# Kernel optimization log

Hardware: AMD Instinct MI355X
Metric: run time of the kernel (lower is better)

## Reference

```python
import jax, jax.numpy as jnp
import numpy as np
import math

T = 2048; HID = 2048; H = 16; KV = 8; G = H // KV; D = 128
GH = 128; BS = 64; NB = T // BS
EPS = 1e-6; RATIO = 0.2; SCALE = 1.0 / math.sqrt(D)


def _rope_tables(length, dim, theta=1000000.0):
    inv = 1.0 / (theta ** (np.arange(0, dim, 2, dtype=np.float32) / dim))
    f = np.outer(np.arange(length, dtype=np.float32), inv)
    emb = np.concatenate([f, f], axis=-1)
    return jnp.asarray(np.cos(emb)), jnp.asarray(np.sin(emb))


def _rot_half(x):
    d = x.shape[-1] // 2
    return jnp.concatenate([-x[..., d:], x[..., :d]], axis=-1)


def _apply_rope(x, cos, sin):
    # x: [T, nH, D], cos/sin: [T, D] broadcast over head dim
    return x * cos[:, None, :] + _rot_half(x) * sin[:, None, :]


def _rmsnorm(x, w, eps=EPS):
    xf = x.astype(jnp.float32)
    v = jnp.mean(xf * xf, axis=-1, keepdims=True)
    return (w * (xf * jax.lax.rsqrt(v + eps))).astype(x.dtype)


def setup_inputs() -> dict:
    key = jax.random.key(0)
    ks = jax.random.split(key, 8)
    s = 0.02
    hidden_states = jax.random.normal(ks[0], (T, HID), jnp.float32)
    Wq = jax.random.normal(ks[1], (HID, H * D), jnp.float32) * s
    Wk = jax.random.normal(ks[2], (HID, KV * D), jnp.float32) * s
    Wv = jax.random.normal(ks[3], (HID, KV * D), jnp.float32) * s
    Wo = jax.random.normal(ks[4], (H * D, HID), jnp.float32) * s
    q_norm_w = jnp.ones((D,), jnp.float32)
    k_norm_w = jnp.ones((D,), jnp.float32)
    gate_wq = jax.random.normal(ks[5], (D, GH), jnp.float32) * s
    gate_wk = jax.random.normal(ks[6], (D, GH), jnp.float32) * s
    cos, sin = _rope_tables(T, D)
    cos_gq, sin_gq = _rope_tables(T, GH)
    cos_blk, sin_blk = _rope_tables(NB, GH)
    # causal block mask: query t may attend to key block j iff j <= t // BS
    block_attention_mask = (jnp.arange(T)[:, None] // BS) >= jnp.arange(NB)[None, :]
    return dict(hidden_states=hidden_states, Wq=Wq, Wk=Wk, Wv=Wv, Wo=Wo,
                q_norm_w=q_norm_w, k_norm_w=k_norm_w, gate_wq=gate_wq, gate_wk=gate_wk,
                cos=cos, sin=sin, cos_gq=cos_gq, sin_gq=sin_gq,
                cos_blk=cos_blk, sin_blk=sin_blk,
                block_attention_mask=block_attention_mask)


def reference(hidden_states, Wq, Wk, Wv, Wo, q_norm_w, k_norm_w, gate_wq, gate_wk,
              cos, sin, cos_gq, sin_gq, cos_blk, sin_blk, block_attention_mask):
    q = (hidden_states @ Wq).reshape(T, H, D)
    k = (hidden_states @ Wk).reshape(T, KV, D)
    v = (hidden_states @ Wv).reshape(T, KV, D)
    q = _rmsnorm(q, q_norm_w)
    k = _rmsnorm(k, k_norm_w)

    # ---- gate network on un-roped q/k: q-head avg-pool to KV heads, k avg-pool per block ----
    q_pool = q.reshape(T, KV, G, D).mean(axis=2)            # [T, KV, D]
    gq = _apply_rope(q_pool @ gate_wq, cos_gq, sin_gq)      # [T, KV, GH]
    k_blk = k.reshape(NB, BS, KV, D).mean(axis=1)           # [NB, KV, D]
    gk = _apply_rope(k_blk @ gate_wk, cos_blk, sin_blk)     # [NB, KV, GH]
    gate_scores = jnp.einsum('tkg,nkg->ktn', gq, gk) / math.sqrt(GH)  # [KV, T, NB]
    predict_mask = jnp.where(block_attention_mask[None], gate_scores, -1e9)

    # ---- main attention (RoPE + GQA causal softmax attention) ----
    qr = _apply_rope(q, cos, sin)
    kr = _apply_rope(k, cos, sin)
    kr_rep = jnp.repeat(kr, G, axis=1)                      # [T, H, D]
    v_rep = jnp.repeat(v, G, axis=1)
    logits = jnp.einsum('thd,shd->hts', qr, kr_rep) * SCALE  # [H, T, T]
    causal = jnp.tril(jnp.ones((T, T), bool))
    logits = jnp.where(causal[None], logits, -jnp.inf)
    probs = jax.nn.softmax(logits, axis=-1)
    attn_output = jnp.einsum('hts,shd->thd', probs, v_rep).reshape(T, H * D) @ Wo

    # ---- pooled ground-truth block mask: attention mass per key block ----
    pooled = probs.reshape(H, T, NB, BS).sum(axis=-1)        # [H, T, NB]
    gt = pooled.reshape(KV, G, T, NB).max(axis=1)            # max_pool3d over head groups -> [KV,T,NB]
    gt = jnp.where(block_attention_mask[None], gt, 0.0)
    gt = gt / (gt.sum(axis=-1, keepdims=True) + 1e-9)

    # ---- KLDiv gate loss on the tail slice (bsz = 1) ----
    start = int(T * RATIO)
    tgt = gt[:, start:, :]                                   # [KV, L, NB]
    logp = jax.nn.log_softmax(predict_mask[:, start:, :], axis=-1)
    safe_t = jnp.where(tgt > 0, tgt, 1.0)
    kl = jnp.where(tgt > 0, tgt * (jnp.log(safe_t) - logp), 0.0)
    gate_loss = kl.reshape(KV, -1).mean(axis=-1).sum()       # KLDivLoss(reduction='mean') per kv head, summed, /bsz(=1)
    return attn_output, gate_loss
```

## Files before the change

### kernel.cpp

```cpp
#include <hip/hip_runtime.h>

#define T_ 2048
#define HID_ 2048
#define H_ 16
#define KV_ 8
#define G_ 2
#define D_ 128
#define GH_ 128
#define BS_ 64
#define NB_ 32
#define START_ 409
#define TG0_ 384
#define SCALE_ 0.08838834764831845f
#define MFIX_ 8.0f

typedef __attribute__((ext_vector_type(8))) short short8_t;
typedef __attribute__((ext_vector_type(4))) float float4_t;
typedef __attribute__((ext_vector_type(8))) unsigned short ushort8_t;
typedef __attribute__((ext_vector_type(4))) unsigned short ushort4_t;

__device__ __forceinline__ float wave_sum(float v) {
#pragma unroll
  for (int o = 32; o > 0; o >>= 1) v += __shfl_xor(v, o, 64);
  return v;
}
__device__ __forceinline__ unsigned short f2bf(float x) {
  unsigned int u = __float_as_uint(x);
  unsigned int r = (u + 0x7fffu + ((u >> 16) & 1u)) >> 16;
  return (unsigned short)r;
}

__device__ __forceinline__ void gload16(const void* g, void* l) {
  __builtin_amdgcn_global_load_lds((const __attribute__((address_space(1))) unsigned int*)g,
                                   (__attribute__((address_space(3))) unsigned int*)l, 16, 0, 0);
}

__device__ __forceinline__ void castT_dev(const float* __restrict__ in,
                                          unsigned short* __restrict__ out, int K, int N,
                                          int ldin, int bx, int by,
                                          unsigned short (*tile)[72], int tid) {
  int k0 = by * 64, n0 = bx * 64;
  int tx = tid & 63, ty4 = tid >> 6;
#pragma unroll
  for (int i = 0; i < 16; ++i) {
    int ky = ty4 * 16 + i;
    tile[tx][ky] = f2bf(in[(size_t)(k0 + ky) * ldin + n0 + tx]);
  }
  __syncthreads();
#pragma unroll
  for (int i = 0; i < 16; ++i) {
    int ny = ty4 * 16 + i;
    out[(size_t)(n0 + ny) * K + k0 + tx] = tile[ny][tx];
  }
}

__global__ __launch_bounds__(256) void castT(const float* __restrict__ in,
                                             unsigned short* __restrict__ out,
                                             int K, int N, int ldin) {
  __shared__ unsigned short tile[64][72];
  castT_dev(in, out, K, N, ldin, blockIdx.x, blockIdx.y, tile, threadIdx.x);
}

__global__ __launch_bounds__(256) void prep_cast(const float* __restrict__ hs,
                                                 const float* __restrict__ Wq,
                                                 const float* __restrict__ Wk,
                                                 const float* __restrict__ Wv,
                                                 const float* __restrict__ Wo,
                                                 const float* __restrict__ gwq,
                                                 const float* __restrict__ gwk,
                                                 unsigned short* __restrict__ hsb,
                                                 unsigned short* __restrict__ WqkvT,
                                                 unsigned short* __restrict__ WoT,
                                                 unsigned short* __restrict__ gwqT,
                                                 unsigned short* __restrict__ gwkT) {
  __shared__ unsigned short tile[64][72];
  int id = blockIdx.x, tid = threadIdx.x;
  if (id < 4096) {
    int i = id * 256 + tid;
    float4 v = ((const float4*)hs)[i];
    ushort4_t o = {f2bf(v.x), f2bf(v.y), f2bf(v.z), f2bf(v.w)};
    *(ushort4_t*)(hsb + (size_t)i * 4) = o;
  } else if (id < 5120) {
    int t = id - 4096;
    castT_dev(Wq, WqkvT, 2048, 2048, 2048, t & 31, t >> 5, tile, tid);
  } else if (id < 5632) {
    int t = id - 5120;
    castT_dev(Wk, WqkvT + (size_t)2048 * 2048, 2048, 1024, 1024, t & 15, t >> 4, tile, tid);
  } else if (id < 6144) {
    int t = id - 5632;
    castT_dev(Wv, WqkvT + (size_t)3072 * 2048, 2048, 1024, 1024, t & 15, t >> 4, tile, tid);
  } else if (id < 7168) {
    int t = id - 6144;
    castT_dev(Wo, WoT, 2048, 2048, 2048, t & 31, t >> 5, tile, tid);
  } else if (id < 7172) {
    int t = id - 7168;
    castT_dev(gwq, gwqT, 128, 128, 128, t & 1, t >> 1, tile, tid);
  } else {
    int t = id - 7172;
    castT_dev(gwk, gwkT, 128, 128, 128, t & 1, t >> 1, tile, tid);
  }
}

__device__ __forceinline__ void gemm_body(const unsigned short* __restrict__ A,
                                          const unsigned short* __restrict__ Bt,
                                          float* __restrict__ C,
                                          int M, int N, int K, int ldc, int bx, int by,
                                          unsigned short* As, unsigned short* Bs) {
  int tid = threadIdx.x;
  int wid = tid >> 6, lane = tid & 63;
  int quad = lane >> 4, l16 = lane & 15;
  int wm = wid & 1, wn = wid >> 1;
  int m0 = by * 128, n0 = bx * 128;
  const unsigned short* gA[4];
  const unsigned short* gB[4];
#pragma unroll
  for (int it = 0; it < 4; ++it) {
    int line = wid * 32 + it * 8 + (lane >> 3);
    int chunk = (lane & 7) ^ (line & 7);
    gA[it] = A + (size_t)(m0 + line) * K + chunk * 8;
    gB[it] = Bt + (size_t)(n0 + line) * K + chunk * 8;
  }
  float4_t acc[4][4];
#pragma unroll
  for (int i = 0; i < 4; ++i)
#pragma unroll
    for (int j = 0; j < 4; ++j) acc[i][j] = (float4_t){0.f, 0.f, 0.f, 0.f};
  int nk = K >> 6;
#pragma unroll
  for (int it = 0; it < 4; ++it) {
    gload16(gA[it], As + (wid * 32 + it * 8) * 64);
    gload16(gB[it], Bs + (wid * 32 + it * 8) * 64);
  }
  for (int t = 0; t < nk; ++t) {
    __syncthreads();
    if (t + 1 < nk) {
      int bo = ((t + 1) & 1) * 8192;
#pragma unroll
      for (int it = 0; it < 4; ++it) {
        gload16(gA[it] + (t + 1) * 64, As + bo + (wid * 32 + it * 8) * 64);
        gload16(gB[it] + (t + 1) * 64, Bs + bo + (wid * 32 + it * 8) * 64);
      }
    }
    const unsigned short* Asc = As + (t & 1) * 8192;
    const unsigned short* Bsc = Bs + (t & 1) * 8192;
    short8_t a[2][4], b[2][4];
#pragma unroll
    for (int ks = 0; ks < 2; ++ks) {
      int sw = ((ks * 4 + quad) ^ (l16 & 7)) * 8;
#pragma unroll
      for (int i = 0; i < 4; ++i) {
        a[ks][i] = *(const short8_t*)&Asc[(wm * 64 + i * 16 + l16) * 64 + sw];
        b[ks][i] = *(const short8_t*)&Bsc[(wn * 64 + i * 16 + l16) * 64 + sw];
      }
    }
#pragma unroll
    for (int ks = 0; ks < 2; ++ks)
#pragma unroll
      for (int i = 0; i < 4; ++i)
#pragma unroll
        for (int j = 0; j < 4; ++j)
          acc[i][j] = __builtin_amdgcn_mfma_f32_16x16x32_bf16(a[ks][i], b[ks][j], acc[i][j], 0, 0, 0);
  }
#pragma unroll
  for (int i = 0; i < 4; ++i)
#pragma unroll
    for (int j = 0; j < 4; ++j)
#pragma unroll
      for (int reg = 0; reg < 4; ++reg)
        C[(size_t)(m0 + wm * 64 + i * 16 + quad * 4 + reg) * ldc + n0 + wn * 64 + j * 16 + l16] =
            acc[i][j][reg];
}

__global__ __launch_bounds__(256) void gemm_bf16_v3(const unsigned short* __restrict__ A,
                                                    const unsigned short* __restrict__ Bt,
                                                    float* __restrict__ C,
                                                    int M, int N, int K, int ldc) {
  __shared__ unsigned short As[2 * 128 * 64];
  __shared__ unsigned short Bs[2 * 128 * 64];
  gemm_body(A, Bt, C, M, N, K, ldc, blockIdx.x, blockIdx.y, As, Bs);
}

__global__ __launch_bounds__(256) void gemm_gates(const unsigned short* __restrict__ Aq,
                                                  const unsigned short* __restrict__ Bq,
                                                  float* __restrict__ Cq,
                                                  const unsigned short* __restrict__ Ak,
                                                  const unsigned short* __restrict__ Bk,
                                                  float* __restrict__ Ck) {
  __shared__ unsigned short As[2 * 128 * 64];
  __shared__ unsigned short Bs[2 * 128 * 64];
  int y = blockIdx.y;
  if (y < 104)
    gemm_body(Aq, Bq, Cq, 13312, 128, 128, 128, 0, y, As, Bs);
  else
    gemm_body(Ak, Bk, Ck, 256, 128, 128, 128, 0, y - 104, As, Bs);
}

__global__ __launch_bounds__(128) void norm_rope_fused(const float* __restrict__ qkvf,
                                                       const float* __restrict__ qw,
                                                       const float* __restrict__ kw,
                                                       const float* __restrict__ cosT,
                                                       const float* __restrict__ sinT,
                                                       unsigned short* __restrict__ qbf,
                                                       unsigned short* __restrict__ qpool_bf,
                                                       unsigned short* __restrict__ kbf,
                                                       float* __restrict__ knorm) {
  int t = blockIdx.x, d = threadIdx.x;
  if (blockIdx.y < 8) {
    int kv = blockIdx.y;
    size_t i0 = (size_t)t * 4096 + (kv * G_) * D_ + d;
    float x0 = qkvf[i0], x1 = qkvf[i0 + D_];
    __shared__ float sred[2][2];
    float s0 = wave_sum(x0 * x0), s1 = wave_sum(x1 * x1);
    if ((d & 63) == 0) { sred[0][d >> 6] = s0; sred[1][d >> 6] = s1; }
    __syncthreads();
    float wv = qw[d];
    float n0 = x0 * rsqrtf((sred[0][0] + sred[0][1]) * (1.f / D_) + 1e-6f) * wv;
    float n1 = x1 * rsqrtf((sred[1][0] + sred[1][1]) * (1.f / D_) + 1e-6f) * wv;
    if (t >= TG0_) qpool_bf[((size_t)(t - TG0_) * KV_ + kv) * D_ + d] = f2bf(0.5f * (n0 + n1));
    __shared__ float sh[2][D_];
    sh[0][d] = n0; sh[1][d] = n1;
    __syncthreads();
    float c = cosT[t * D_ + d], s = sinT[t * D_ + d];
    float r0 = (d < 64) ? -sh[0][d + 64] : sh[0][d - 64];
    float r1 = (d < 64) ? -sh[1][d + 64] : sh[1][d - 64];
    qbf[((size_t)(t * H_) + kv * G_) * D_ + d] = f2bf(n0 * c + r0 * s);
    qbf[((size_t)(t * H_) + kv * G_ + 1) * D_ + d] = f2bf(n1 * c + r1 * s);
  } else {
    int kv = blockIdx.y - 8;
    float x = qkvf[(size_t)t * 4096 + 2048 + kv * D_ + d];
    __shared__ float sredk[2];
    float s0 = wave_sum(x * x);
    if ((d & 63) == 0) sredk[d >> 6] = s0;
    __syncthreads();
    float nk = x * rsqrtf((sredk[0] + sredk[1]) * (1.f / D_) + 1e-6f) * kw[d];
    knorm[(size_t)(t * KV_ + kv) * D_ + d] = nk;
    __shared__ float shk[D_];
    shk[d] = nk;
    __syncthreads();
    float rot = (d < 64) ? -shk[d + 64] : shk[d - 64];
    kbf[(size_t)(t * KV_ + kv) * D_ + d] = f2bf(nk * cosT[t * D_ + d] + rot * sinT[t * D_ + d]);
  }
}

__global__ __launch_bounds__(128) void kblk_kernel(const float* __restrict__ knorm,
                                                   unsigned short* __restrict__ kblk_bf) {
  int n = blockIdx.x, kv = blockIdx.y, d = threadIdx.x;
  float s = 0.f;
  for (int i = 0; i < BS_; ++i) s += knorm[((size_t)(n * BS_ + i) * KV_ + kv) * D_ + d];
  kblk_bf[(size_t)(n * KV_ + kv) * D_ + d] = f2bf(s * (1.f / BS_));
}

__global__ __launch_bounds__(128) void rope_g_fused(float* __restrict__ gq, float* __restrict__ gk,
                                                    const float* __restrict__ cosG,
                                                    const float* __restrict__ sinG,
                                                    const float* __restrict__ cosB,
                                                    const float* __restrict__ sinB) {
  int r = blockIdx.x, kvh = blockIdx.y, d = threadIdx.x;
  float* x;
  size_t base;
  float c_, s_;
  if (r < NB_) {
    x = gk;
    base = (size_t)(r * KV_ + kvh) * GH_;
    c_ = cosB[r * GH_ + d]; s_ = sinB[r * GH_ + d];
  } else {
    int rr = r - NB_;
    x = gq;
    base = (size_t)(rr * KV_ + kvh) * GH_;
    c_ = cosG[(size_t)(TG0_ + rr) * GH_ + d]; s_ = sinG[(size_t)(TG0_ + rr) * GH_ + d];
  }
  __shared__ float sh[GH_];
  sh[d] = x[base + d];
  __syncthreads();
  float rot = (d < 64) ? -sh[d + 64] : sh[d - 64];
  x[base + d] = sh[d] * c_ + rot * s_;
}

__global__ __launch_bounds__(256, 2) void attn_mfma(const unsigned short* __restrict__ qbf,
                                                    const unsigned short* __restrict__ kbf,
                                                    const unsigned short* __restrict__ vt,
                                                    float* __restrict__ pooled,
                                                    float* __restrict__ o_acc,
                                                    float* __restrict__ l_acc) {
  int kv = blockIdx.x;
  int yy = blockIdx.y;
  int tile, c_lo, c_hi;
  if (yy < 32) { tile = yy;      c_lo = 0;                c_hi = (tile + 2) >> 1; }
  else         { tile = 63 - yy; c_lo = (tile + 2) >> 1;  c_hi = tile + 1; }
  int t0 = tile * 64;
  int tid = threadIdx.x;
  int wid = tid >> 6, lane = tid & 63;
  int quad = lane >> 4, l16 = lane & 15;
  __shared__ unsigned short Ks[2][64 * 128];
  __shared__ unsigned short Vs[2][128 * 64];
  __shared__ unsigned short Ps[8][16 * 64];

  const unsigned short* kbase[4];
  const unsigned short* vbase[4];
#pragma unroll
  for (int it = 0; it < 4; ++it) {
    int seg = wid * 4 + it;
    int krow = seg * 4 + (lane >> 4);
    int kchk = lane & 15;
    kbase[it] = kbf + ((size_t)krow * KV_ + kv) * D_ + ((kchk ^ (krow & 7)) << 3);
    int vrow = seg * 8 + (lane >> 3);
    int vchk = lane & 7;
    vbase[it] = vt + (size_t)(kv * 128 + vrow) * T_ + ((vchk ^ (vrow & 7)) << 3);
  }

  int tq = t0 + wid * 16 + l16;
  short8_t qf[2][4];
#pragma unroll
  for (int hh = 0; hh < 2; ++hh)
#pragma unroll
    for (int kb = 0; kb < 4; ++kb)
      qf[hh][kb] = *(const short8_t*)&qbf[((size_t)tq * H_ + kv * G_ + hh) * D_ + kb * 32 + quad * 8];

  const short one_bf = (short)0x3F80;
  short8_t ones = {one_bf, one_bf, one_bf, one_bf, one_bf, one_bf, one_bf, one_bf};

  int tbase = t0 + wid * 16 + quad * 4;
  float l_[2][4] = {};
  float pacc[2][2][4] = {};
  float4_t o[2][8];
#pragma unroll
  for (int hh = 0; hh < 2; ++hh)
#pragma unroll
    for (int j = 0; j < 8; ++j) o[hh][j] = (float4_t){0.f, 0.f, 0.f, 0.f};

#pragma unroll
  for (int it = 0; it < 4; ++it) {
    gload16(kbase[it] + (size_t)c_lo * 65536, &Ks[c_lo & 1][(wid * 4 + it) * 512]);
    gload16(vbase[it] + c_lo * 64, &Vs[c_lo & 1][(wid * 4 + it) * 512]);
  }
  for (int c = c_lo; c < c_hi; ++c) {
    __syncthreads();
    if (c + 1 < c_hi) {
      int b = (c + 1) & 1;
#pragma unroll
      for (int it = 0; it < 4; ++it) {
        gload16(kbase[it] + (size_t)(c + 1) * 65536, &Ks[b][(wid * 4 + it) * 512]);
        gload16(vbase[it] + (c + 1) * 64, &Vs[b][(wid * 4 + it) * 512]);
      }
    }
    const unsigned short* Ksc = Ks[c & 1];
    const unsigned short* Vsc = Vs[c & 1];
    int half = c >> 4, cl = c & 15;

    float4_t s[2][4];
#pragma unroll
    for (int j = 0; j < 4; ++j) {
      float4_t a0 = (float4_t){0.f, 0.f, 0.f, 0.f};
      float4_t a1 = (float4_t){0.f, 0.f, 0.f, 0.f};
#pragma unroll
      for (int kb = 0; kb < 4; ++kb) {
        short8_t kf = *(const short8_t*)&Ksc[(j * 16 + l16) * 128 + (((kb * 4 + quad) ^ (l16 & 7)) << 3)];
        a0 = __builtin_amdgcn_mfma_f32_16x16x32_bf16(qf[0][kb], kf, a0, 0, 0, 0);
        a1 = __builtin_amdgcn_mfma_f32_16x16x32_bf16(qf[1][kb], kf, a1, 0, 0, 0);
      }
      s[0][j] = a0;
      s[1][j] = a1;
    }
#pragma unroll
    for (int hh = 0; hh < 2; ++hh) {
      if (c == tile) {
#pragma unroll
        for (int reg = 0; reg < 4; ++reg) {
          int trow = tbase + reg;
#pragma unroll
          for (int j = 0; j < 4; ++j) {
            float p = __expf(s[hh][j][reg] * SCALE_ - MFIX_);
            s[hh][j][reg] = (c * 64 + j * 16 + l16 <= trow) ? p : 0.f;
          }
        }
      } else {
#pragma unroll
        for (int j = 0; j < 4; ++j)
#pragma unroll
          for (int reg = 0; reg < 4; ++reg)
            s[hh][j][reg] = __expf(s[hh][j][reg] * SCALE_ - MFIX_);
      }
#pragma unroll
      for (int j = 0; j < 4; ++j)
#pragma unroll
        for (int reg = 0; reg < 4; ++reg) {
          int r = quad * 4 + reg;
          Ps[wid * 2 + hh][r * 64 + ((j * 16 + l16) ^ ((r & 7) << 3))] = f2bf(s[hh][j][reg]);
        }
    }
    float4_t pool[2] = {(float4_t){0.f, 0.f, 0.f, 0.f}, (float4_t){0.f, 0.f, 0.f, 0.f}};
#pragma unroll
    for (int ks = 0; ks < 2; ++ks) {
      int psw = l16 * 64 + (((ks * 4 + quad) ^ (l16 & 7)) << 3);
      short8_t pf0 = *(const short8_t*)&Ps[wid * 2 + 0][psw];
      short8_t pf1 = *(const short8_t*)&Ps[wid * 2 + 1][psw];
      pool[0] = __builtin_amdgcn_mfma_f32_16x16x32_bf16(pf0, ones, pool[0], 0, 0, 0);
      pool[1] = __builtin_amdgcn_mfma_f32_16x16x32_bf16(pf1, ones, pool[1], 0, 0, 0);
#pragma unroll
      for (int jt = 0; jt < 8; ++jt) {
        short8_t vf = *(const short8_t*)&Vsc[(jt * 16 + l16) * 64 + (((ks * 4 + quad) ^ (l16 & 7)) << 3)];
        o[0][jt] = __builtin_amdgcn_mfma_f32_16x16x32_bf16(pf0, vf, o[0][jt], 0, 0, 0);
        o[1][jt] = __builtin_amdgcn_mfma_f32_16x16x32_bf16(pf1, vf, o[1][jt], 0, 0, 0);
      }
    }
#pragma unroll
    for (int hh = 0; hh < 2; ++hh)
#pragma unroll
      for (int reg = 0; reg < 4; ++reg) {
        l_[hh][reg] += pool[hh][reg];
        if (l16 == cl) pacc[hh][half][reg] = pool[hh][reg];
      }
  }
#pragma unroll
  for (int hh = 0; hh < 2; ++hh) {
    int h = kv * G_ + hh;
#pragma unroll
    for (int reg = 0; reg < 4; ++reg) {
      int trow = tbase + reg;
      if (l16 >= c_lo && l16 < c_hi)
        pooled[((size_t)h * T_ + trow) * NB_ + l16] = pacc[hh][0][reg];
      if (16 + l16 >= c_lo && 16 + l16 < c_hi)
        pooled[((size_t)h * T_ + trow) * NB_ + 16 + l16] = pacc[hh][1][reg];
    }
#pragma unroll
    for (int jt = 0; jt < 8; ++jt)
#pragma unroll
      for (int reg = 0; reg < 4; ++reg)
        atomicAdd(&o_acc[(((size_t)h * T_) + tbase + reg) * D_ + jt * 16 + l16], o[hh][jt][reg]);
    if (l16 == 0) {
#pragma unroll
      for (int reg = 0; reg < 4; ++reg)
        atomicAdd(&l_acc[(size_t)h * T_ + tbase + reg], l_[hh][reg]);
    }
  }
}

__global__ __launch_bounds__(256) void attn_combine(const float* __restrict__ o_acc,
                                                    const float* __restrict__ l_acc,
                                                    unsigned short* __restrict__ attnb) {
  int gid = blockIdx.x * 256 + threadIdx.x;
  int row = gid >> 5, q4 = gid & 31;
  int h = row >> 11, t = row & 2047;
  float inv = 1.f / l_acc[row];
  float4 a = ((const float4*)o_acc)[gid];
  ushort4_t ov = {f2bf(a.x * inv), f2bf(a.y * inv), f2bf(a.z * inv), f2bf(a.w * inv)};
  *(ushort4_t*)(attnb + (size_t)t * (H_ * D_) + h * D_ + q4 * 4) = ov;
}

__device__ __forceinline__ void gate_loss_body(const float* __restrict__ gq,
                                               const float* __restrict__ gk,
                                               const float* __restrict__ pooled,
                                               const float* __restrict__ l_acc,
                                               float* __restrict__ klsum,
                                               int kv, int yblk) {
  int sub = threadIdx.x >> 5;
  int n = threadIdx.x & 31;
  int tloc = yblk * 8 + sub;
  bool act = tloc < (T_ - START_);
  int t = START_ + (act ? tloc : 0);
  const float4* a = (const float4*)(gq + ((size_t)(t - TG0_) * KV_ + kv) * GH_);
  const float4* b = (const float4*)(gk + (size_t)(n * KV_ + kv) * GH_);
  float dot = 0.f;
#pragma unroll
  for (int d4 = 0; d4 < 32; ++d4) {
    float4 av = a[d4], bv = b[d4];
    dot += av.x * bv.x + av.y * bv.y + av.z * bv.z + av.w * bv.w;
  }
  bool valid = (t / BS_) >= n;
  float score = valid ? dot * SCALE_ : -1e9f;
  float M = score;
#pragma unroll
  for (int o = 16; o > 0; o >>= 1) M = fmaxf(M, __shfl_xor(M, o, 64));
  float e = __expf(score - M);
  float Z = e;
#pragma unroll
  for (int o = 16; o > 0; o >>= 1) Z += __shfl_xor(Z, o, 64);
  float logZ = M + logf(Z);
  float g = 0.f;
  if (valid) {
    float rl0 = 1.f / l_acc[(size_t)(kv * G_) * T_ + t];
    float rl1 = 1.f / l_acc[(size_t)(kv * G_ + 1) * T_ + t];
    float p0 = pooled[((size_t)(kv * G_) * T_ + t) * NB_ + n] * rl0;
    float p1 = pooled[((size_t)(kv * G_ + 1) * T_ + t) * NB_ + n] * rl1;
    g = fmaxf(p0, p1);
  }
  float gs = g;
#pragma unroll
  for (int o = 16; o > 0; o >>= 1) gs += __shfl_xor(gs, o, 64);
  float tgt = g / (gs + 1e-9f);
  float kl = (tgt > 0.f) ? tgt * (logf(tgt) - (score - logZ)) : 0.f;
  float ks = kl;
#pragma unroll
  for (int o = 16; o > 0; o >>= 1) ks += __shfl_xor(ks, o, 64);
  if (n == 0 && act) klsum[kv * (T_ - START_) + tloc] = ks;
}

__global__ __launch_bounds__(256) void wo_gemm_gate(const unsigned short* __restrict__ A,
                                                    const unsigned short* __restrict__ Bt,
                                                    float* __restrict__ C,
                                                    const float* __restrict__ gq,
                                                    const float* __restrict__ gk,
                                                    const float* __restrict__ pooled,
                                                    const float* __restrict__ l_acc,
                                                    float* __restrict__ klsum) {
  __shared__ unsigned short As[2 * 128 * 64];
  __shared__ unsigned short Bs[2 * 128 * 64];
  if (blockIdx.y < 16) {
    gemm_body(A, Bt, C, 2048, 2048, 2048, 2048, blockIdx.x, blockIdx.y, As, Bs);
  } else {
    int g = blockIdx.x + (blockIdx.y - 16) * 16;
    int kv = g & 7, yblk = g >> 3;
    if (yblk < 205) gate_loss_body(gq, gk, pooled, l_acc, klsum, kv, yblk);
  }
}

__global__ __launch_bounds__(256) void finalize_loss(const float* __restrict__ klsum,
                                                     float* __restrict__ out) {
  const int n = KV_ * (T_ - START_);
  float s = 0.f;
  for (int i = threadIdx.x; i < n; i += 256) s += klsum[i];
  s = wave_sum(s);
  __shared__ float sh[4];
  if ((threadIdx.x & 63) == 0) sh[threadIdx.x >> 6] = s;
  __syncthreads();
  if (threadIdx.x == 0)
    out[0] = (sh[0] + sh[1] + sh[2] + sh[3]) * (1.f / ((float)(T_ - START_) * NB_));
}

extern "C" void kernel_launch(void* const* d_in, const int* in_sizes, int n_in,
                              void* d_out, int out_size, void* d_ws, size_t ws_size,
                              hipStream_t stream) {
  const float* hs   = (const float*)d_in[0];
  const float* Wq   = (const float*)d_in[1];
  const float* Wk   = (const float*)d_in[2];
  const float* Wv   = (const float*)d_in[3];
  const float* Wo   = (const float*)d_in[4];
  const float* qw   = (const float*)d_in[5];
  const float* kw   = (const float*)d_in[6];
  const float* gwq  = (const float*)d_in[7];
  const float* gwk  = (const float*)d_in[8];
  const float* cosT = (const float*)d_in[9];
  const float* sinT = (const float*)d_in[10];
  const float* cosG = (const float*)d_in[11];
  const float* sinG = (const float*)d_in[12];
  const float* cosB = (const float*)d_in[13];
  const float* sinB = (const float*)d_in[14];
  float* out = (float*)d_out;
  float* ws = (float*)d_ws;
  const size_t MEG = 1048576;

  float*          qkvf     = ws;
  unsigned short* attnb    = (unsigned short*)ws;
  float*          pooled   = ws + 2 * MEG;
  float*          klsum    = ws + 3 * MEG;
  float*          l_acc    = ws + 3 * MEG + 65536;
  float*          o_acc    = ws + 4 * MEG;
  unsigned short* WqkvT    = (unsigned short*)(ws + 8 * MEG);
  unsigned short* qbf      = WqkvT;
  unsigned short* kbf      = WqkvT + 4 * MEG;
  unsigned short* vt       = WqkvT + 6 * MEG;
  unsigned short* hsb      = (unsigned short*)(ws + 12 * MEG);
  float*          knorm    = ws + 12 * MEG;
  unsigned short* WoT      = (unsigned short*)(ws + 14 * MEG);
  unsigned short* qpool_bf = (unsigned short*)(ws + 16 * MEG);
  float*          gq       = ws + 17 * MEG;
  unsigned short* kblk_bf  = (unsigned short*)(ws + 18 * MEG + 786432);
  float*          gk       = ws + 18 * MEG + 819200;
  unsigned short* gwqT     = (unsigned short*)(ws + 18 * MEG + 851968);
  unsigned short* gwkT     = (unsigned short*)(ws + 18 * MEG + 860160);

  prep_cast<<<7176, 256, 0, stream>>>(hs, Wq, Wk, Wv, Wo, gwq, gwk, hsb, WqkvT, WoT, gwqT, gwkT);
  gemm_bf16_v3<<<dim3(32, 16), 256, 0, stream>>>(hsb, WqkvT, qkvf, 2048, 4096, 2048, 4096);
  norm_rope_fused<<<dim3(T_, 16), 128, 0, stream>>>(qkvf, qw, kw, cosT, sinT, qbf, qpool_bf,
                                                    kbf, knorm);
  castT<<<dim3(16, 32), 256, 0, stream>>>(qkvf + 3072, vt, T_, 1024, 4096);
  hipMemsetAsync(o_acc, 0, (size_t)4 * MEG * sizeof(float), stream);
  hipMemsetAsync(l_acc, 0, (size_t)H_ * T_ * sizeof(float), stream);
  kblk_kernel<<<dim3(NB_, KV_), 128, 0, stream>>>(knorm, kblk_bf);
  gemm_gates<<<dim3(1, 106), 256, 0, stream>>>(qpool_bf, gwqT, gq, kblk_bf, gwkT, gk);
  rope_g_fused<<<dim3(NB_ + (T_ - TG0_), KV_), 128, 0, stream>>>(gq, gk, cosG, sinG, cosB, sinB);
  attn_mfma<<<dim3(KV_, 64), 256, 0, stream>>>(qbf, kbf, vt, pooled, o_acc, l_acc);
  attn_combine<<<4096, 256, 0, stream>>>(o_acc, l_acc, attnb);
  wo_gemm_gate<<<dim3(16, 119), 256, 0, stream>>>(attnb, WoT, out, gq, gk, pooled, l_acc, klsum);
  finalize_loss<<<1, 256, 0, stream>>>(klsum, out + (size_t)T_ * HID_);
}
```

Measured before the change: 333.1 us.

## Move gate-loss work into combine kernel and stage gk in shared memory

The gate KL-loss blocks move out of the Wo GEMM launch and into the attention-combine launch, so the Wo projection now runs as a plain GEMM. In the gate-loss body, each block first copies the 32x128 gk tile for its kv head into XOR-swizzled shared memory, instead of every thread reading gk from global memory. The intent is to stop the GEMM from sharing its grid with irregular gate blocks, and to overlap the gate work with the memory-bound combine. The cost is an extra shared-memory fill and a barrier per gate block.

```diff
diff --git a/kernel.cpp b/kernel.cpp
--- a/kernel.cpp
+++ b/kernel.cpp
@@ -435,35 +435,32 @@
   }
 }
 
-__global__ __launch_bounds__(256) void attn_combine(const float* __restrict__ o_acc,
-                                                    const float* __restrict__ l_acc,
-                                                    unsigned short* __restrict__ attnb) {
-  int gid = blockIdx.x * 256 + threadIdx.x;
-  int row = gid >> 5, q4 = gid & 31;
-  int h = row >> 11, t = row & 2047;
-  float inv = 1.f / l_acc[row];
-  float4 a = ((const float4*)o_acc)[gid];
-  ushort4_t ov = {f2bf(a.x * inv), f2bf(a.y * inv), f2bf(a.z * inv), f2bf(a.w * inv)};
-  *(ushort4_t*)(attnb + (size_t)t * (H_ * D_) + h * D_ + q4 * 4) = ov;
-}
-
 __device__ __forceinline__ void gate_loss_body(const float* __restrict__ gq,
                                                const float* __restrict__ gk,
                                                const float* __restrict__ pooled,
                                                const float* __restrict__ l_acc,
                                                float* __restrict__ klsum,
-                                               int kv, int yblk) {
-  int sub = threadIdx.x >> 5;
-  int n = threadIdx.x & 31;
+                                               int kv, int yblk, float4* gks4) {
+  int tid = threadIdx.x;
+#pragma unroll
+  for (int p = 0; p < 4; ++p) {
+    int f = p * 256 + tid;
+    int n = f >> 5, d4 = f & 31;
+    gks4[n * 32 + (d4 ^ (n & 7))] =
+        *(const float4*)(gk + ((size_t)n * KV_ + kv) * GH_ + d4 * 4);
+  }
+  __syncthreads();
+  int sub = tid >> 5;
+  int n = tid & 31;
   int tloc = yblk * 8 + sub;
   bool act = tloc < (T_ - START_);
   int t = START_ + (act ? tloc : 0);
   const float4* a = (const float4*)(gq + ((size_t)(t - TG0_) * KV_ + kv) * GH_);
-  const float4* b = (const float4*)(gk + (size_t)(n * KV_ + kv) * GH_);
   float dot = 0.f;
 #pragma unroll
   for (int d4 = 0; d4 < 32; ++d4) {
-    float4 av = a[d4], bv = b[d4];
+    float4 av = a[d4];
+    float4 bv = gks4[n * 32 + (d4 ^ (n & 7))];
     dot += av.x * bv.x + av.y * bv.y + av.z * bv.z + av.w * bv.w;
   }
   bool valid = (t / BS_) >= n;
@@ -495,22 +492,25 @@
   if (n == 0 && act) klsum[kv * (T_ - START_) + tloc] = ks;
 }
 
-__global__ __launch_bounds__(256) void wo_gemm_gate(const unsigned short* __restrict__ A,
-                                                    const unsigned short* __restrict__ Bt,
-                                                    float* __restrict__ C,
+__global__ __launch_bounds__(256) void combine_gate(const float* __restrict__ o_acc,
+                                                    const float* __restrict__ l_acc,
+                                                    unsigned short* __restrict__ attnb,
                                                     const float* __restrict__ gq,
                                                     const float* __restrict__ gk,
                                                     const float* __restrict__ pooled,
-                                                    const float* __restrict__ l_acc,
                                                     float* __restrict__ klsum) {
-  __shared__ unsigned short As[2 * 128 * 64];
-  __shared__ unsigned short Bs[2 * 128 * 64];
-  if (blockIdx.y < 16) {
-    gemm_body(A, Bt, C, 2048, 2048, 2048, 2048, blockIdx.x, blockIdx.y, As, Bs);
+  __shared__ float4 gks4[1024];
+  int id = blockIdx.x;
+  if (id < 1640) {
+    gate_loss_body(gq, gk, pooled, l_acc, klsum, id & 7, id >> 3, gks4);
   } else {
-    int g = blockIdx.x + (blockIdx.y - 16) * 16;
-    int kv = g & 7, yblk = g >> 3;
-    if (yblk < 205) gate_loss_body(gq, gk, pooled, l_acc, klsum, kv, yblk);
+    int gid = (id - 1640) * 256 + threadIdx.x;
+    int row = gid >> 5, q4 = gid & 31;
+    int h = row >> 11, t = row & 2047;
+    float inv = 1.f / l_acc[row];
+    float4 a = ((const float4*)o_acc)[gid];
+    ushort4_t ov = {f2bf(a.x * inv), f2bf(a.y * inv), f2bf(a.z * inv), f2bf(a.w * inv)};
+    *(ushort4_t*)(attnb + (size_t)t * (H_ * D_) + h * D_ + q4 * 4) = ov;
   }
 }
 
@@ -580,7 +580,7 @@
   gemm_gates<<<dim3(1, 106), 256, 0, stream>>>(qpool_bf, gwqT, gq, kblk_bf, gwkT, gk);
   rope_g_fused<<<dim3(NB_ + (T_ - TG0_), KV_), 128, 0, stream>>>(gq, gk, cosG, sinG, cosB, sinB);
   attn_mfma<<<dim3(KV_, 64), 256, 0, stream>>>(qbf, kbf, vt, pooled, o_acc, l_acc);
-  attn_combine<<<4096, 256, 0, stream>>>(o_acc, l_acc, attnb);
-  wo_gemm_gate<<<dim3(16, 119), 256, 0, stream>>>(attnb, WoT, out, gq, gk, pooled, l_acc, klsum);
+  combine_gate<<<1640 + 4096, 256, 0, stream>>>(o_acc, l_acc, attnb, gq, gk, pooled, klsum);
+  gemm_bf16_v3<<<dim3(16, 16), 256, 0, stream>>>(attnb, WoT, out, 2048, 2048, 2048, 2048);
   finalize_loss<<<1, 256, 0, stream>>>(klsum, out + (size_t)T_ * HID_);
 }
```

Measured after the change: 321.4 us. -3.5%, faster.
